# Kernel optimization log

Hardware: AMD Instinct MI355X
Metric: run time of the kernel (lower is better)

Reference implementation:

```python
import jax, jax.numpy as jnp
import numpy as np

N, V = 2048, 32000


def setup_inputs() -> dict:
    key = jax.random.key(0)
    k1, k2 = jax.random.split(key)
    logits = jax.random.normal(k1, (N, V), jnp.float32) * 4.0
    # pre-drawn Gumbel noise => categorical sample via argmax(logits + gumbel)
    u = jax.random.uniform(k2, (N, V), jnp.float32, minval=1e-6, maxval=1.0 - 1e-6)
    gumbel = -jnp.log(-jnp.log(u))
    return {
        "logits": logits,
        "gumbel": gumbel,
        "temperature": jnp.float32(0.7),
        "top_p": jnp.float32(0.95),
        "top_k": 50,
        "accept_threshold": jnp.float32(0.9),
    }


def reference(logits, gumbel, temperature, top_p, top_k, accept_threshold):
    neg_inf = jnp.finfo(logits.dtype).min
    x = logits / temperature  # temperature > 0 path

    # --- top_p_logits: sort desc, cumsum of softmax, shift-by-one keep-top mask ---
    order = jnp.argsort(-x, axis=-1)                       # [N, V] descending order
    sorted_x = jnp.take_along_axis(x, order, axis=-1)
    cum = jnp.cumsum(jax.nn.softmax(sorted_x, axis=-1), axis=-1)
    remove_sorted = cum > top_p
    # shift right by one, always keep top-1 token
    remove_sorted = jnp.concatenate(
        [jnp.zeros_like(remove_sorted[..., :1]), remove_sorted[..., :-1]], axis=-1)
    inv = jnp.argsort(order, axis=-1)                      # inverse permutation
    remove = jnp.take_along_axis(remove_sorted, inv, axis=-1)
    x = jnp.where(remove, neg_inf, x)

    # --- top_k_logits: mask everything below the k-th largest ---
    kth = jax.lax.top_k(x, top_k)[0][..., -1:]             # [N, 1]
    x = jnp.where(x < kth, neg_inf, x)

    # --- softmax + categorical sample (Gumbel-argmax) + confidence ---
    probs = jax.nn.softmax(x, axis=-1)                     # [N, V]
    x0 = jnp.argmax(x + gumbel, axis=-1)                   # [N] sampled tokens
    initial_confidence = jnp.take_along_axis(probs, x0[:, None], axis=-1)[:, 0]
    confidence = initial_confidence                        # default (no margin/neg_entropy)

    # --- accept loop: accept above threshold; if none, accept top-1 confidence ---
    high = initial_confidence > accept_threshold           # [N] bool
    any_high = jnp.any(high)
    fallback = jnp.zeros_like(high).at[jnp.argmax(confidence)].set(True)
    accepted = jnp.where(any_high, high, fallback)

    return confidence, x0, initial_confidence, accepted
```

## Files before the change

### kernel.cpp

```cpp
#include <hip/hip_runtime.h>
#include <math.h>
#include <float.h>

#define VOCAB    32000
#define NT       256
#define NWAVES   (NT / 64)
#define CAP      1024
#define KMAX     64
#define KREF     24.0f
#define THETA0   14.0f
#define LOG2E    1.4426950408889634f
#define THT      ((THETA0 - KREF) * LOG2E)
#define FBDELTA  (12.0f * LOG2E)
#define NCHUNK   (VOCAB / 4)
#define DEPTH    4

typedef float vf4 __attribute__((ext_vector_type(4)));
typedef const __attribute__((address_space(1))) void g1v;
typedef __attribute__((address_space(3))) void l3v;


#define PROCESS(v, jj)                                                              \
    {                                                                               \
        float t0 = fmaf((v).x, a, b);                                               \
        float t1 = fmaf((v).y, a, b);                                               \
        float t2 = fmaf((v).z, a, b);                                               \
        float t3 = fmaf((v).w, a, b);                                               \
        sA += exp2f(t0);                                                            \
        sB += exp2f(t1);                                                            \
        sA += exp2f(t2);                                                            \
        sB += exp2f(t3);                                                            \
        tmax = fmaxf(tmax, fmaxf(fmaxf(t0, t1), fmaxf(t2, t3)));                    \
        int bi = (jj) * 4;                                                          \
        if (t0 > THT) { int p = atomicAdd(&s_cnt, 1); if (p < CAP) { s_val[p] = (v).x / T; s_idx[p] = bi;     } } \
        if (t1 > THT) { int p = atomicAdd(&s_cnt, 1); if (p < CAP) { s_val[p] = (v).y / T; s_idx[p] = bi + 1; } } \
        if (t2 > THT) { int p = atomicAdd(&s_cnt, 1); if (p < CAP) { s_val[p] = (v).z / T; s_idx[p] = bi + 2; } } \
        if (t3 > THT) { int p = atomicAdd(&s_cnt, 1); if (p < CAP) { s_val[p] = (v).w / T; s_idx[p] = bi + 3; } } \
    }

#define ISSUE(k)                                                                    \
    {                                                                               \
        const float* gp = logits + base + 4u * ((size_t)(wid + 4 * (k)) * 64 + lane); \
        __builtin_amdgcn_global_load_lds((g1v*)gp,                                  \
            (l3v*)&stage[(wid << 10) + (((k) & 3) << 8)], 16, 0, 0);                \
    }

#define CONSUME(i)                                                                  \
    {                                                                               \
        vf4 v = *(const vf4*)&stage[(wid << 10) + (((i) & 3) << 8) + (lane << 2)];  \
        PROCESS(v, (wid + 4 * (i)) * 64 + lane);                                    \
    }

__global__ __launch_bounds__(NT, 6) void dream_row_kernel(
    const float* __restrict__ logits,
    const float* __restrict__ gumbel,
    const float* __restrict__ tempP,
    const float* __restrict__ toppP,
    const int*   __restrict__ topkP,
    float* __restrict__ out_conf,
    float* __restrict__ out_x0,
    float* __restrict__ out_iconf)
{
    const int row = blockIdx.x;
    const int tid = threadIdx.x;
    const int lane = tid & 63;
    const int wid  = tid >> 6;
    const size_t base = (size_t)row * VOCAB;
    const float T = tempP[0];
    const float a = (1.0f / T) * LOG2E;
    const float b = -(KREF * LOG2E);

    __shared__ float stage[NT * DEPTH * 4];
    __shared__ float s_val[CAP];
    __shared__ int   s_idx[CAP];
    __shared__ int   s_cnt;
    __shared__ float wsum[NWAVES], wmax[NWAVES];
    __shared__ float sh_S, sh_m;
    __shared__ float so_val[KMAX];
    __shared__ int   so_idx[KMAX];
    __shared__ int   sh_nk;
    __shared__ float sh_skept;

    if (tid == 0) s_cnt = 0;
    __syncthreads();

    float sA = 0.0f, sB = 0.0f;
    float tmax = -FLT_MAX;
    const int nq = (wid == 0) ? 32 : 31;

    asm volatile("s_waitcnt vmcnt(0)" ::: "memory");
    ISSUE(0); ISSUE(1); ISSUE(2); ISSUE(3);

    for (int i = 0; i + 4 < nq; ++i) {
        asm volatile("s_waitcnt vmcnt(3)" ::: "memory");
        __builtin_amdgcn_sched_barrier(0);
        CONSUME(i);
        asm volatile("s_waitcnt lgkmcnt(0)" ::: "memory");
        __builtin_amdgcn_sched_barrier(0);
        ISSUE(i + 4);
    }
    asm volatile("s_waitcnt vmcnt(3)" ::: "memory"); __builtin_amdgcn_sched_barrier(0); CONSUME(nq - 4);
    asm volatile("s_waitcnt vmcnt(2)" ::: "memory"); __builtin_amdgcn_sched_barrier(0); CONSUME(nq - 3);
    asm volatile("s_waitcnt vmcnt(1)" ::: "memory"); __builtin_amdgcn_sched_barrier(0); CONSUME(nq - 2);
    asm volatile("s_waitcnt vmcnt(0)" ::: "memory"); __builtin_amdgcn_sched_barrier(0); CONSUME(nq - 1);

    float s = sA + sB;
    float mx = tmax;
    #pragma unroll
    for (int o = 32; o > 0; o >>= 1) {
        s  += __shfl_down(s, o, 64);
        mx  = fmaxf(mx, __shfl_down(mx, o, 64));
    }
    if (lane == 0) { wsum[wid] = s; wmax[wid] = mx; }
    __syncthreads();
    if (tid == 0) {
        float St = 0.0f, Mt = -FLT_MAX;
        #pragma unroll
        for (int w = 0; w < NWAVES; ++w) { St += wsum[w]; Mt = fmaxf(Mt, wmax[w]); }
        sh_S = St; sh_m = Mt;
    }
    __syncthreads();
    const float S_K = sh_S;
    const float m_t = sh_m;
    int C = min(s_cnt, CAP);

    if (C < KMAX) {
        if (tid == 0) s_cnt = 0;
        __syncthreads();
        const float th2t = m_t - FBDELTA;
        const vf4* l4 = (const vf4*)(logits + base);
        for (int j = tid; j < NCHUNK; j += NT) {
            vf4 v = l4[j];
            float t0 = fmaf(v.x, a, b);
            float t1 = fmaf(v.y, a, b);
            float t2 = fmaf(v.z, a, b);
            float t3 = fmaf(v.w, a, b);
            int bi = j * 4;
            if (t0 > th2t) { int p = atomicAdd(&s_cnt, 1); if (p < CAP) { s_val[p] = v.x / T; s_idx[p] = bi;     } }
            if (t1 > th2t) { int p = atomicAdd(&s_cnt, 1); if (p < CAP) { s_val[p] = v.y / T; s_idx[p] = bi + 1; } }
            if (t2 > th2t) { int p = atomicAdd(&s_cnt, 1); if (p < CAP) { s_val[p] = v.z / T; s_idx[p] = bi + 2; } }
            if (t3 > th2t) { int p = atomicAdd(&s_cnt, 1); if (p < CAP) { s_val[p] = v.w / T; s_idx[p] = bi + 3; } }
        }
        __syncthreads();
        C = min(s_cnt, CAP);
    }

    for (int c = tid; c < C; c += NT) {
        float vc = s_val[c]; int ic = s_idx[c];
        int r = 0;
        #pragma unroll 4
        for (int j = 0; j < C; ++j) {
            float vj = s_val[j];
            if (vj > vc || (vj == vc && s_idx[j] < ic)) r++;
        }
        if (r < KMAX) { so_val[r] = vc; so_idx[r] = ic; }
    }
    __syncthreads();

    if (tid == 0) {
        int k = topkP[0]; if (k > KMAX) k = KMAX; if (k < 1) k = 1;
        const float topp = toppP[0];
        const int lim = min(C, k);
        float cum = 0.0f;
        float skept = 0.0f;
        int nk = 0;
        for (int j = 0; j < lim; ++j) {
            if (cum > topp) break;
            float e = exp2f(fmaf(so_val[j], LOG2E, b));
            cum += e / S_K;
            skept += e;
            nk++;
        }
        sh_nk = nk;
        sh_skept = skept;
    }
    __syncthreads();
    const int nk = sh_nk;
    const float skept = sh_skept;

    if (wid == 0) {
        float bv = -FLT_MAX; int bi = 0x7FFFFFFF; float bx = 0.0f;
        if (lane < nk) {
            int gi = so_idx[lane];
            bx = so_val[lane];
            bv = bx + gumbel[base + gi];
            bi = gi;
        }
        #pragma unroll
        for (int o = 32; o > 0; o >>= 1) {
            float ov = __shfl_down(bv, o, 64);
            int   oi = __shfl_down(bi, o, 64);
            float ox = __shfl_down(bx, o, 64);
            if (ov > bv || (ov == bv && oi < bi)) { bv = ov; bi = oi; bx = ox; }
        }
        if (lane == 0) {
            float eb = exp2f(fmaf(bx, LOG2E, b));
            float confv = eb / skept;
            out_conf[row]  = confv;
            out_x0[row]    = (float)bi;
            out_iconf[row] = confv;
        }
    }
}

__global__ __launch_bounds__(NT) void accept_kernel(
    const float* __restrict__ conf,
    const float* __restrict__ thrP,
    float* __restrict__ acc_out,
    int N)
{
    __shared__ float rv[NT];
    __shared__ int   ri[NT];
    __shared__ int   ra[NT];
    const int tid = threadIdx.x;
    const float thr = thrP[0];

    float bv = -FLT_MAX; int bi = 0x7FFFFFFF; int any = 0;
    for (int i = tid; i < N; i += NT) {
        float v = conf[i];
        if (v > thr) any = 1;
        if (v > bv) { bv = v; bi = i; }
    }
    rv[tid] = bv; ri[tid] = bi; ra[tid] = any;
    __syncthreads();
    #pragma unroll
    for (int s = NT / 2; s > 0; s >>= 1) {
        if (tid < s) {
            float ov = rv[tid + s]; int oi = ri[tid + s];
            if (ov > rv[tid] || (ov == rv[tid] && oi < ri[tid])) {
                rv[tid] = ov; ri[tid] = oi;
            }
            ra[tid] |= ra[tid + s];
        }
        __syncthreads();
    }
    const int anyHigh = ra[0];
    const int amax = ri[0];
    for (int i = tid; i < N; i += NT) {
        float a;
        if (anyHigh) a = (conf[i] > thr) ? 1.0f : 0.0f;
        else         a = (i == amax) ? 1.0f : 0.0f;
        acc_out[i] = a;
    }
}

extern "C" void kernel_launch(void* const* d_in, const int* in_sizes, int n_in,
                              void* d_out, int out_size, void* d_ws, size_t ws_size,
                              hipStream_t stream)
{
    const float* logits = (const float*)d_in[0];
    const float* gumbel = (const float*)d_in[1];
    const float* tempP  = (const float*)d_in[2];
    const float* toppP  = (const float*)d_in[3];
    const int*   topkP  = (const int*)d_in[4];
    const float* thrP   = (const float*)d_in[5];
    float* out = (float*)d_out;
    const int N = in_sizes[0] / VOCAB;

    dream_row_kernel<<<N, NT, 0, stream>>>(
        logits, gumbel, tempP, toppP, topkP,
        out , out + N , out + 2 * N );

    accept_kernel<<<1, NT, 0, stream>>>(
        out, thrP, out + 3 * N , N);
}
```

Measured before the change: 547.0 us.

## Replace LDS-staged async loads with register double-buffered nontemporal loads

Drops the global_load_lds staging pipeline, which waited on vmcnt and went through a 4-deep LDS buffer, in favour of two register banks of six float4 loads each. Each bank is consumed while the other is in flight, all fully unrolled. Loads also become nontemporal, including in the fallback rescan. This removes the LDS round trip and its waitcnt stalls and frees the staging shared memory. In exchange it uses more VGPRs (24 float4 live), which under launch bounds of 6 could spill or lower occupancy.

```diff
diff --git a/kernel.cpp b/kernel.cpp
--- a/kernel.cpp
+++ b/kernel.cpp
@@ -13,11 +13,8 @@
 #define THT      ((THETA0 - KREF) * LOG2E)
 #define FBDELTA  (12.0f * LOG2E)
 #define NCHUNK   (VOCAB / 4)
-#define DEPTH    4
 
 typedef float vf4 __attribute__((ext_vector_type(4)));
-typedef const __attribute__((address_space(1))) void g1v;
-typedef __attribute__((address_space(3))) void l3v;
 
 
 #define PROCESS(v, jj)                                                              \
@@ -38,18 +35,23 @@
         if (t3 > THT) { int p = atomicAdd(&s_cnt, 1); if (p < CAP) { s_val[p] = (v).w / T; s_idx[p] = bi + 3; } } \
     }
 
-#define ISSUE(k)                                                                    \
-    {                                                                               \
-        const float* gp = logits + base + 4u * ((size_t)(wid + 4 * (k)) * 64 + lane); \
-        __builtin_amdgcn_global_load_lds((g1v*)gp,                                  \
-            (l3v*)&stage[(wid << 10) + (((k) & 3) << 8)], 16, 0, 0);                \
-    }
-
-#define CONSUME(i)                                                                  \
-    {                                                                               \
-        vf4 v = *(const vf4*)&stage[(wid << 10) + (((i) & 3) << 8) + (lane << 2)];  \
-        PROCESS(v, (wid + 4 * (i)) * 64 + lane);                                    \
-    }
+#define LOAD6(g, i0)                                                                \
+    g##0 = __builtin_nontemporal_load(&l4[tid + ((i0) + 0) * NT]);                  \
+    g##1 = __builtin_nontemporal_load(&l4[tid + ((i0) + 1) * NT]);                  \
+    g##2 = __builtin_nontemporal_load(&l4[tid + ((i0) + 2) * NT]);                  \
+    g##3 = __builtin_nontemporal_load(&l4[tid + ((i0) + 3) * NT]);                  \
+    g##4 = __builtin_nontemporal_load(&l4[tid + ((i0) + 4) * NT]);                  \
+    g##5 = __builtin_nontemporal_load(&l4[tid + ((i0) + 5) * NT]);
+
+#define CONSUME6(g, i0)                                                             \
+    PROCESS(g##0, tid + ((i0) + 0) * NT);                                           \
+    PROCESS(g##1, tid + ((i0) + 1) * NT);                                           \
+    PROCESS(g##2, tid + ((i0) + 2) * NT);                                           \
+    PROCESS(g##3, tid + ((i0) + 3) * NT);                                           \
+    PROCESS(g##4, tid + ((i0) + 4) * NT);                                           \
+    PROCESS(g##5, tid + ((i0) + 5) * NT);
+
+#define SB  __builtin_amdgcn_sched_barrier(0)
 
 __global__ __launch_bounds__(NT, 6) void dream_row_kernel(
     const float* __restrict__ logits,
@@ -66,11 +68,11 @@
     const int lane = tid & 63;
     const int wid  = tid >> 6;
     const size_t base = (size_t)row * VOCAB;
+    const vf4* l4 = (const vf4*)(logits + base);
     const float T = tempP[0];
     const float a = (1.0f / T) * LOG2E;
     const float b = -(KREF * LOG2E);
 
-    __shared__ float stage[NT * DEPTH * 4];
     __shared__ float s_val[CAP];
     __shared__ int   s_idx[CAP];
     __shared__ int   s_cnt;
@@ -86,23 +88,30 @@
 
     float sA = 0.0f, sB = 0.0f;
     float tmax = -FLT_MAX;
-    const int nq = (wid == 0) ? 32 : 31;
-
-    asm volatile("s_waitcnt vmcnt(0)" ::: "memory");
-    ISSUE(0); ISSUE(1); ISSUE(2); ISSUE(3);
-
-    for (int i = 0; i + 4 < nq; ++i) {
-        asm volatile("s_waitcnt vmcnt(3)" ::: "memory");
-        __builtin_amdgcn_sched_barrier(0);
-        CONSUME(i);
-        asm volatile("s_waitcnt lgkmcnt(0)" ::: "memory");
-        __builtin_amdgcn_sched_barrier(0);
-        ISSUE(i + 4);
-    }
-    asm volatile("s_waitcnt vmcnt(3)" ::: "memory"); __builtin_amdgcn_sched_barrier(0); CONSUME(nq - 4);
-    asm volatile("s_waitcnt vmcnt(2)" ::: "memory"); __builtin_amdgcn_sched_barrier(0); CONSUME(nq - 3);
-    asm volatile("s_waitcnt vmcnt(1)" ::: "memory"); __builtin_amdgcn_sched_barrier(0); CONSUME(nq - 2);
-    asm volatile("s_waitcnt vmcnt(0)" ::: "memory"); __builtin_amdgcn_sched_barrier(0); CONSUME(nq - 1);
+    vf4 a0, a1, a2, a3, a4, a5;
+    vf4 b0, b1, b2, b3, b4, b5;
+
+    LOAD6(a, 0);
+    LOAD6(b, 6);
+    SB;
+    CONSUME6(a, 0);
+    LOAD6(a, 12);
+    SB;
+    CONSUME6(b, 6);
+    LOAD6(b, 18);
+    SB;
+    CONSUME6(a, 12);
+    LOAD6(a, 24);
+    SB;
+    CONSUME6(b, 18);
+    vf4 c0 = __builtin_nontemporal_load(&l4[tid + 30 * NT]);
+    const int hasTail = (tid + 31 * NT) < NCHUNK;
+    vf4 c1;
+    if (hasTail) c1 = __builtin_nontemporal_load(&l4[tid + 31 * NT]);
+    SB;
+    CONSUME6(a, 24);
+    PROCESS(c0, tid + 30 * NT);
+    if (hasTail) { PROCESS(c1, tid + 31 * NT); }
 
     float s = sA + sB;
     float mx = tmax;
@@ -128,9 +137,8 @@
         if (tid == 0) s_cnt = 0;
         __syncthreads();
         const float th2t = m_t - FBDELTA;
-        const vf4* l4 = (const vf4*)(logits + base);
         for (int j = tid; j < NCHUNK; j += NT) {
-            vf4 v = l4[j];
+            vf4 v = __builtin_nontemporal_load(&l4[j]);
             float t0 = fmaf(v.x, a, b);
             float t1 = fmaf(v.y, a, b);
             float t2 = fmaf(v.z, a, b);
```

New measurement: 551.3 us. No clear change (+0.8%).

## Replace LDS-staged async loads with batched nontemporal direct register loads

Applied to the files above, without the earlier changes.

Removes the global_load_lds staging buffer and its manual vmcnt/lgkmcnt pipeline. Each wave now streams a contiguous quarter of the row straight into registers, eight 16-byte nontemporal loads at a time. Dropping the stage buffer frees LDS, and launch bounds rise from 6 to 8 blocks per CU for more occupancy. This costs more registers for the eight in-flight vectors and gives up the explicit software pipelining, so latency hiding now relies on occupancy.

```diff
diff --git a/kernel.cpp b/kernel.cpp
--- a/kernel.cpp
+++ b/kernel.cpp
@@ -13,11 +13,9 @@
 #define THT      ((THETA0 - KREF) * LOG2E)
 #define FBDELTA  (12.0f * LOG2E)
 #define NCHUNK   (VOCAB / 4)
-#define DEPTH    4
+#define QUART    2048
 
 typedef float vf4 __attribute__((ext_vector_type(4)));
-typedef const __attribute__((address_space(1))) void g1v;
-typedef __attribute__((address_space(3))) void l3v;
 
 
 #define PROCESS(v, jj)                                                              \
@@ -38,20 +36,7 @@
         if (t3 > THT) { int p = atomicAdd(&s_cnt, 1); if (p < CAP) { s_val[p] = (v).w / T; s_idx[p] = bi + 3; } } \
     }
 
-#define ISSUE(k)                                                                    \
-    {                                                                               \
-        const float* gp = logits + base + 4u * ((size_t)(wid + 4 * (k)) * 64 + lane); \
-        __builtin_amdgcn_global_load_lds((g1v*)gp,                                  \
-            (l3v*)&stage[(wid << 10) + (((k) & 3) << 8)], 16, 0, 0);                \
-    }
-
-#define CONSUME(i)                                                                  \
-    {                                                                               \
-        vf4 v = *(const vf4*)&stage[(wid << 10) + (((i) & 3) << 8) + (lane << 2)];  \
-        PROCESS(v, (wid + 4 * (i)) * 64 + lane);                                    \
-    }
-
-__global__ __launch_bounds__(NT, 6) void dream_row_kernel(
+__global__ __launch_bounds__(NT, 8) void dream_row_kernel(
     const float* __restrict__ logits,
     const float* __restrict__ gumbel,
     const float* __restrict__ tempP,
@@ -66,11 +51,11 @@
     const int lane = tid & 63;
     const int wid  = tid >> 6;
     const size_t base = (size_t)row * VOCAB;
+    const vf4* l4 = (const vf4*)(logits + base);
     const float T = tempP[0];
     const float a = (1.0f / T) * LOG2E;
     const float b = -(KREF * LOG2E);
 
-    __shared__ float stage[NT * DEPTH * 4];
     __shared__ float s_val[CAP];
     __shared__ int   s_idx[CAP];
     __shared__ int   s_cnt;
@@ -86,23 +71,34 @@
 
     float sA = 0.0f, sB = 0.0f;
     float tmax = -FLT_MAX;
-    const int nq = (wid == 0) ? 32 : 31;
-
-    asm volatile("s_waitcnt vmcnt(0)" ::: "memory");
-    ISSUE(0); ISSUE(1); ISSUE(2); ISSUE(3);
-
-    for (int i = 0; i + 4 < nq; ++i) {
-        asm volatile("s_waitcnt vmcnt(3)" ::: "memory");
-        __builtin_amdgcn_sched_barrier(0);
-        CONSUME(i);
-        asm volatile("s_waitcnt lgkmcnt(0)" ::: "memory");
-        __builtin_amdgcn_sched_barrier(0);
-        ISSUE(i + 4);
-    }
-    asm volatile("s_waitcnt vmcnt(3)" ::: "memory"); __builtin_amdgcn_sched_barrier(0); CONSUME(nq - 4);
-    asm volatile("s_waitcnt vmcnt(2)" ::: "memory"); __builtin_amdgcn_sched_barrier(0); CONSUME(nq - 3);
-    asm volatile("s_waitcnt vmcnt(1)" ::: "memory"); __builtin_amdgcn_sched_barrier(0); CONSUME(nq - 2);
-    asm volatile("s_waitcnt vmcnt(0)" ::: "memory"); __builtin_amdgcn_sched_barrier(0); CONSUME(nq - 1);
+    const int q  = wid * QUART;
+    const int nk = (wid == 3) ? 29 : 32;
+
+    int k = 0;
+    #pragma unroll 1
+    for (; k + 8 <= nk; k += 8) {
+        vf4 r0 = __builtin_nontemporal_load(&l4[q + (k + 0) * 64 + lane]);
+        vf4 r1 = __builtin_nontemporal_load(&l4[q + (k + 1) * 64 + lane]);
+        vf4 r2 = __builtin_nontemporal_load(&l4[q + (k + 2) * 64 + lane]);
+        vf4 r3 = __builtin_nontemporal_load(&l4[q + (k + 3) * 64 + lane]);
+        vf4 r4 = __builtin_nontemporal_load(&l4[q + (k + 4) * 64 + lane]);
+        vf4 r5 = __builtin_nontemporal_load(&l4[q + (k + 5) * 64 + lane]);
+        vf4 r6 = __builtin_nontemporal_load(&l4[q + (k + 6) * 64 + lane]);
+        vf4 r7 = __builtin_nontemporal_load(&l4[q + (k + 7) * 64 + lane]);
+        PROCESS(r0, q + (k + 0) * 64 + lane);
+        PROCESS(r1, q + (k + 1) * 64 + lane);
+        PROCESS(r2, q + (k + 2) * 64 + lane);
+        PROCESS(r3, q + (k + 3) * 64 + lane);
+        PROCESS(r4, q + (k + 4) * 64 + lane);
+        PROCESS(r5, q + (k + 5) * 64 + lane);
+        PROCESS(r6, q + (k + 6) * 64 + lane);
+        PROCESS(r7, q + (k + 7) * 64 + lane);
+    }
+    #pragma unroll 1
+    for (; k < nk; ++k) {
+        vf4 v = __builtin_nontemporal_load(&l4[q + k * 64 + lane]);
+        PROCESS(v, q + k * 64 + lane);
+    }
 
     float s = sA + sB;
     float mx = tmax;
@@ -128,9 +124,8 @@
         if (tid == 0) s_cnt = 0;
         __syncthreads();
         const float th2t = m_t - FBDELTA;
-        const vf4* l4 = (const vf4*)(logits + base);
         for (int j = tid; j < NCHUNK; j += NT) {
-            vf4 v = l4[j];
+            vf4 v = __builtin_nontemporal_load(&l4[j]);
             float t0 = fmaf(v.x, a, b);
             float t1 = fmaf(v.y, a, b);
             float t2 = fmaf(v.z, a, b);
@@ -158,29 +153,29 @@
     __syncthreads();
 
     if (tid == 0) {
-        int k = topkP[0]; if (k > KMAX) k = KMAX; if (k < 1) k = 1;
+        int k2 = topkP[0]; if (k2 > KMAX) k2 = KMAX; if (k2 < 1) k2 = 1;
         const float topp = toppP[0];
-        const int lim = min(C, k);
+        const int lim = min(C, k2);
         float cum = 0.0f;
         float skept = 0.0f;
-        int nk = 0;
+        int nk2 = 0;
         for (int j = 0; j < lim; ++j) {
             if (cum > topp) break;
             float e = exp2f(fmaf(so_val[j], LOG2E, b));
             cum += e / S_K;
             skept += e;
-            nk++;
-        }
-        sh_nk = nk;
+            nk2++;
+        }
+        sh_nk = nk2;
         sh_skept = skept;
     }
     __syncthreads();
-    const int nk = sh_nk;
+    const int nkk = sh_nk;
     const float skept = sh_skept;
 
     if (wid == 0) {
         float bv = -FLT_MAX; int bi = 0x7FFFFFFF; float bx = 0.0f;
-        if (lane < nk) {
+        if (lane < nkk) {
             int gi = so_idx[lane];
             bx = so_val[lane];
             bv = bx + gumbel[base + gi];
```

Result: faster. 505.6 us (-7.6%).
